# Kernel tuning notes

Hardware: AMD Instinct MI355X
Metric: run time of the kernel (lower is better)

The kernel has to match this reference:

```python
import jax, jax.numpy as jnp
import numpy as np
from jax import lax

T, B = 32, 256
C1, C2, C3 = 64, 128, 256
CDECAY, VDECAY, VTH, GRAD_WIN = 0.5, 0.75, 0.5, 0.3

# PseudoSpikeRect: hard threshold fwd, rectangular surrogate grad bwd
@jax.custom_vjp
def spike(v):
    return (v > VTH).astype(v.dtype)

def _spk_fwd(v):
    return spike(v), v

def _spk_bwd(v, g):
    return (g * (jnp.abs(v - VTH) < GRAD_WIN).astype(g.dtype),)

spike.defvjp(_spk_fwd, _spk_bwd)


def conv2d(x, w, b):
    y = lax.conv_general_dilated(x, w, (1, 1), 'VALID',
                                 dimension_numbers=('NCHW', 'OIHW', 'NCHW'))
    return y + b[None, :, None, None]


def lin(x, w, b):
    return x @ w.T + b


def lif(z, state):
    # CUBA-LIF cell: current decay + input psp, voltage decay with reset-by-spike
    spk, cur, vlt = state[0], state[1], state[2]
    cur = CDECAY * cur + z
    vlt = VDECAY * vlt * (1.0 - spk) + cur
    out = spike(vlt)
    return out, jnp.stack([out, cur, vlt])


def setup_inputs() -> dict:
    key = jax.random.key(0)
    ks = jax.random.split(key, 10)
    f32 = jnp.float32
    def rnd(k, shape, fan_in):
        return jax.random.normal(k, shape, f32) / np.sqrt(fan_in)
    return {
        'input_data': jax.random.normal(ks[0], (B, 1, 10, 10, T), f32),
        'conv1_w': rnd(ks[1], (C1, 1, 3, 3), 9),
        'conv1_b': jnp.zeros((C1,), f32),
        'conv2_w': rnd(ks[2], (C2, C1, 3, 3), 9 * C1),
        'conv2_b': jnp.zeros((C2,), f32),
        'conv3_w': rnd(ks[3], (C3, C2, 3, 3), 9 * C2),
        'conv3_b': jnp.zeros((C3,), f32),
        'tc_w': rnd(ks[4], (3, C3, C3), C3),
        'tc_b': jnp.zeros((3, C3), f32),
        'rec_w': rnd(ks[5], (C3, C3), C3),
        'rec_b': jnp.zeros((C3,), f32),
        'fc1_w': rnd(ks[6], (128, C3), C3),
        'fc1_b': jnp.zeros((128,), f32),
        'fc2_w': rnd(ks[7], (2, 128), 128),
        'ts_weights': jnp.ones((T, 1), f32) / T,
        'st_c1': jnp.zeros((3, B, C1, 8, 8), f32),
        'st_c2': jnp.zeros((3, B, C2, 6, 6), f32),
        'st_c3': jnp.zeros((3, B, C3, 1, 1), f32),
        'st_tc1': jnp.zeros((3, B, C3), f32),
        'st_r1': jnp.zeros((3, B, C3), f32),
        'st_f1': jnp.zeros((3, B, 128), f32),
    }


def reference(input_data, conv1_w, conv1_b, conv2_w, conv2_b, conv3_w, conv3_b,
              tc_w, tc_b, rec_w, rec_b, fc1_w, fc1_b, fc2_w, ts_weights,
              st_c1, st_c2, st_c3, st_tc1, st_r1, st_f1):
    xs = jnp.moveaxis(input_data, -1, 0)  # [T, B, 1, 10, 10]
    buf0 = jnp.zeros((3, B, C3), xs.dtype)  # temporal-conv spike buffer, oldest first

    # temporal conv: at step t only min(t+1,3) buffered spikes exist; psp_func j
    # applies to the j-th oldest buffered spike (buffer newest at index 2).
    def tc_len1(buf):
        return lin(buf[2], tc_w[0], tc_b[0])
    def tc_len2(buf):
        return lin(buf[1], tc_w[0], tc_b[0]) + lin(buf[2], tc_w[1], tc_b[1])
    def tc_len3(buf):
        return (lin(buf[0], tc_w[0], tc_b[0]) + lin(buf[1], tc_w[1], tc_b[1])
                + lin(buf[2], tc_w[2], tc_b[2]))

    def step(carry, inp):
        s1, s2, s3, stc, sr, sf, buf, acc = carry
        x, tw, t = inp
        c1, s1 = lif(conv2d(x, conv1_w, conv1_b), s1)
        c2, s2 = lif(conv2d(c1, conv2_w, conv2_b), s2)
        pooled = c2.reshape(B, C2, 3, 2, 3, 2).mean(axis=(3, 5))  # AvgPool2d(2)
        c3, s3 = lif(conv2d(pooled, conv3_w, conv3_b), s3)
        flat = c3.reshape(B, C3)
        buf = jnp.concatenate([buf[1:], flat[None]], axis=0)
        psp = lax.switch(jnp.minimum(t, 2), [tc_len1, tc_len2, tc_len3], buf)
        tc, stc = lif(psp, stc)
        r, sr = lif(tc + lin(sr[0], rec_w, rec_b), sr)  # recurrent: Identity psp + rec(pre_spike)
        f1, sf = lif(lin(r, fc1_w, fc1_b), sf)
        acc = acc + (f1 @ fc2_w.T) * tw
        return (s1, s2, s3, stc, sr, sf, buf, acc), None

    init = (st_c1, st_c2, st_c3, st_tc1, st_r1, st_f1, buf0,
            jnp.zeros((B, 2), xs.dtype))
    carry, _ = lax.scan(step, init, (xs, ts_weights[:, 0], jnp.arange(T)))
    return carry[-1]
```

## Files before the change

kernel.cpp:

```cpp
#include <hip/hip_runtime.h>

#define T 32
#define B 256

typedef int v4i __attribute__((ext_vector_type(4)));

#define OFF_BD2   0
#define OFF_BD3   368640
#define OFF_BDTC  1843200
#define OFF_BDF1  2826240
#define OFF_BDREC 2990080
#define OFF_S1    3514368
#define OFF_POOL  37068800
#define OFF_PSP3  46505984
#define OFF_S3    63283200
#define OFF_PSPTC 65380352
#define OFF_TC    82157568
#define OFF_R     84254720
#define OFF_PSPF1 OFF_PSPTC

__global__ __launch_bounds__(256) void k_prepd(const float* __restrict__ c2w,
        const float* __restrict__ c3w, const float* __restrict__ tcw,
        const float* __restrict__ f1w, const float* __restrict__ rcw,
        signed char* __restrict__ Bd2, signed char* __restrict__ Bd3,
        signed char* __restrict__ Bdtc, signed char* __restrict__ Bdf1,
        signed char* __restrict__ Bdrec) {
    int idx = blockIdx.x * 256 + threadIdx.x;
    float w; signed char* base; int plane, off;
    if (idx < 73728) {
        int oc = idx / 576, kpos = idx - oc * 576;
        int kk = kpos >> 6, ic = kpos & 63;
        int ky = kk / 3, kx = kk - ky * 3;
        w = c2w[((oc * 64 + ic) * 3 + ky) * 3 + kx];
        base = Bd2; plane = 73728; off = (kk * 128 + oc) * 64 + ic;
    } else if (idx < 368640) {
        int m = idx - 73728;
        int oc = m / 1152, kpos = m - oc * 1152;
        int win = kpos >> 7, ic = kpos & 127;
        w = c3w[(oc * 128 + ic) * 9 + win];
        base = Bd3; plane = 294912;
        off = ((kpos >> 6) * 256 + oc) * 64 + (kpos & 63);
    } else if (idx < 565248) {
        int m = idx - 368640;
        int oc = m / 768, kpos = m - oc * 768;
        int j = kpos >> 8, kc = kpos & 255;
        w = tcw[(j * 256 + oc) * 256 + kc];
        base = Bdtc; plane = 196608;
        off = ((kpos >> 6) * 256 + oc) * 64 + (kpos & 63);
    } else if (idx < 598016) {
        int m = idx - 565248;
        int oc = m >> 8, kc = m & 255;
        w = f1w[oc * 256 + kc];
        base = Bdf1; plane = 32768;
        off = ((kc >> 6) * 128 + oc) * 64 + (kc & 63);
    } else if (idx < 663552) {
        int m = idx - 598016;
        int oc = m >> 8, k = m & 255;
        w = rcw[oc * 256 + k];
        base = Bdrec; plane = 65536; off = m;
    } else return;
    long long W = (long long)rint((double)w * 2147483648.0);
#pragma unroll
    for (int d = 0; d < 3; ++d) {
        int dig = (int)(((W + 128) & 255) - 128);
        base[d * plane + off] = (signed char)dig;
        W = (W - dig) >> 8;
    }
    base[3 * plane + off] = (signed char)W;
}

__global__ __launch_bounds__(256) void k_conv1(const float* __restrict__ x,
        const float* __restrict__ w1, const float* __restrict__ b1,
        unsigned char* __restrict__ s1) {
    __shared__ float xl[3200];
    int b  = blockIdx.x >> 2;
    int bp = blockIdx.x & 3;
    int oc = threadIdx.x & 63;
    int sub = threadIdx.x >> 6;
    const float* xb = x + b * 3200;
    for (int i = threadIdx.x; i < 3200; i += 256)
        xl[(i & 31) * 100 + (i >> 5)] = xb[i];
    double wd[9];
#pragma unroll
    for (int j = 0; j < 9; ++j) wd[j] = (double)w1[oc * 9 + j];
    double bias = (double)b1[oc];
    __syncthreads();
    double cur[4], vlt[4];
    unsigned spkb = 0;
#pragma unroll
    for (int i = 0; i < 4; ++i) { cur[i] = 0.0; vlt[i] = 0.0; }
    const int pixbase = bp * 16 + sub * 4;
    for (int t = 0; t < T; ++t) {
#pragma unroll
        for (int i = 0; i < 4; ++i) {
            int pix = pixbase + i;
            int oy = pix >> 3, ox = pix & 7;
            const float* xt = &xl[t * 100 + oy * 10 + ox];
            double z = bias;
#pragma unroll
            for (int ky = 0; ky < 3; ++ky)
#pragma unroll
                for (int kx = 0; kx < 3; ++kx)
                    z = fma(wd[ky * 3 + kx], (double)xt[ky * 10 + kx], z);
            cur[i] = 0.5 * cur[i] + z;
            int s = (spkb >> i) & 1;
            vlt[i] = (s ? 0.0 : 0.75 * vlt[i]) + cur[i];
            s = (vlt[i] > 0.5) ? 1 : 0;
            spkb = (spkb & ~(1u << i)) | ((unsigned)s << i);
            s1[((size_t)(t * B + b) * 64 + pix) * 64 + oc] = (unsigned char)s;
        }
    }
}

__global__ __launch_bounds__(256, 2) void k_conv2(const unsigned char* __restrict__ s1,
        const signed char* __restrict__ Bd2, const float* __restrict__ cb2,
        unsigned char* __restrict__ pooled) {
    __shared__ __align__(16) unsigned char As[32 * 1024];
    __shared__ unsigned smask[4][64];
    const int b = blockIdx.x / 9;
    const int w = blockIdx.x - b * 9;
    const int wy = w / 3, wx = w - wy * 3;
    const int tid = threadIdx.x;
    const int wave = tid >> 6, lane = tid & 63;
    const int col = lane & 15, quad = lane >> 4;
    const int m = lane & 15;
    const int px = m >> 2, tq = m & 3;
    const int py0 = px >> 1, px0 = px & 1;

    {
        const int pixbase = (2 * wy) * 8 + 2 * wx;
        for (int c = tid; c < 2048; c += 256) {
            int t = c >> 6, rem = c & 63;
            int p = rem & 15, qo = rem >> 4;
            int ly = p >> 2, lx = p & 3;
            int pix = pixbase + ly * 8 + lx;
            v4i v = *(const v4i*)(s1 + (((size_t)(t * B + b) * 64 + pix) << 6) + qo * 16);
            *(v4i*)(As + t * 1024 + ((qo * 16) + (p ^ (2 * (t & 3)))) * 16) = v;
        }
    }
    __syncthreads();

    for (int nh = 0; nh < 2; ++nh) {
        const int oc = nh * 64 + wave * 16 + col;
        const int boff = oc * 64 + quad * 16;
        v4i acc[8][4];
#pragma unroll
        for (int mt = 0; mt < 8; ++mt)
#pragma unroll
            for (int d = 0; d < 4; ++d) acc[mt][d] = (v4i){0, 0, 0, 0};
        v4i Bc[4], Bn[4];
#pragma unroll
        for (int d = 0; d < 4; ++d)
            Bc[d] = *(const v4i*)(Bd2 + (size_t)d * 73728 + boff);
#pragma unroll 1
        for (int kk = 0; kk < 9; ++kk) {
            if (kk < 8) {
#pragma unroll
                for (int d = 0; d < 4; ++d)
                    Bn[d] = *(const v4i*)(Bd2 + (size_t)d * 73728 + (kk + 1) * 8192 + boff);
            }
            const int ky = kk / 3, kx = kk - ky * 3;
            const int p = (py0 + ky) * 4 + (px0 + kx);
            const unsigned char* Ab = As + tq * 1024 + (quad * 16 + (p ^ (2 * tq))) * 16;
#pragma unroll
            for (int mt = 0; mt < 8; ++mt) {
                v4i Af = *(const v4i*)(Ab + mt * 4096);
#pragma unroll
                for (int d = 0; d < 4; ++d)
                    acc[mt][d] = __builtin_amdgcn_mfma_i32_16x16x64_i8(Af, Bc[d], acc[mt][d], 0, 0, 0);
            }
            if (kk < 8) {
#pragma unroll
                for (int d = 0; d < 4; ++d) Bc[d] = Bn[d];
            }
        }
        double cur = 0.0, vlt = 0.0;
        int spk = 0;
        unsigned bits = 0;
        double bias = (double)cb2[oc];
#pragma unroll
        for (int mt = 0; mt < 8; ++mt)
#pragma unroll
            for (int r = 0; r < 4; ++r) {
                double v = (double)acc[mt][3][r];
                v = fma(v, 256.0, (double)acc[mt][2][r]);
                v = fma(v, 256.0, (double)acc[mt][1][r]);
                v = fma(v, 256.0, (double)acc[mt][0][r]);
                double z = fma(v, 0x1p-31, bias);
                cur = 0.5 * cur + z;
                vlt = (spk ? 0.0 : 0.75 * vlt) + cur;
                spk = (vlt > 0.5) ? 1 : 0;
                bits |= ((unsigned)spk) << (mt * 4 + r);
            }
        smask[quad][wave * 16 + col] = bits;
        __syncthreads();
        {
            unsigned m0 = smask[0][wave * 16 + col], m1 = smask[1][wave * 16 + col];
            unsigned m2 = smask[2][wave * 16 + col], m3 = smask[3][wave * 16 + col];
#pragma unroll
            for (int q = 0; q < 8; ++q) {
                int t = quad * 8 + q;
                unsigned s = ((m0 >> t) & 1) + ((m1 >> t) & 1) + ((m2 >> t) & 1) + ((m3 >> t) & 1);
                pooled[(size_t)((w * 32 + t) * 256 + b) * 128 + oc] = (unsigned char)s;
            }
        }
        __syncthreads();
    }
}

__global__ __launch_bounds__(256) void k_c3psp(const unsigned char* __restrict__ pooled,
        const signed char* __restrict__ Bd3, const float* __restrict__ b3,
        double* __restrict__ psp) {
    __shared__ __align__(16) unsigned char As[32 * 1168];
    const int mt = blockIdx.x, rbase = mt * 32;
    const int tid = threadIdx.x;
    const int wave = tid >> 6, lane = tid & 63;
    const int col = lane & 15, quad = lane >> 4;
    for (int c = tid; c < 2304; c += 256) {
        int row = c / 72, cho = c - row * 72;
        int wn = cho >> 3, ico = (cho & 7) * 16;
        v4i v = *(const v4i*)(pooled + ((size_t)(wn * 8192) + rbase + row) * 128 + ico);
        *(v4i*)(As + row * 1168 + cho * 16) = v;
    }
    __syncthreads();
    const int nb = wave * 64;
    const double scl[4] = { 0x1p-33, 0x1p-25, 0x1p-17, 0x1p-9 };
    double psum[2][4][4];
#pragma unroll
    for (int ml = 0; ml < 2; ++ml)
#pragma unroll
        for (int nt = 0; nt < 4; ++nt)
#pragma unroll
            for (int r = 0; r < 4; ++r) psum[ml][nt][r] = 0.0;
    for (int d = 0; d < 4; ++d) {
        v4i acc[2][4];
#pragma unroll
        for (int ml = 0; ml < 2; ++ml)
#pragma unroll
            for (int nt = 0; nt < 4; ++nt) acc[ml][nt] = (v4i){0, 0, 0, 0};
        v4i Bc[4], Bn[4];
#pragma unroll
        for (int nt = 0; nt < 4; ++nt)
            Bc[nt] = *(const v4i*)(Bd3 + (((size_t)(d * 18) * 256
                        + nb + nt * 16 + col) << 6) + quad * 16);
#pragma unroll 1
        for (int kk = 0; kk < 18; ++kk) {
            if (kk < 17) {
#pragma unroll
                for (int nt = 0; nt < 4; ++nt)
                    Bn[nt] = *(const v4i*)(Bd3 + (((size_t)(d * 18 + kk + 1) * 256
                                + nb + nt * 16 + col) << 6) + quad * 16);
            }
#pragma unroll
            for (int ml = 0; ml < 2; ++ml) {
                v4i Af = *(const v4i*)(As + (ml * 16 + col) * 1168 + kk * 64 + quad * 16);
#pragma unroll
                for (int nt = 0; nt < 4; ++nt)
                    acc[ml][nt] = __builtin_amdgcn_mfma_i32_16x16x64_i8(Af, Bc[nt], acc[ml][nt], 0, 0, 0);
            }
            if (kk < 17) {
#pragma unroll
                for (int nt = 0; nt < 4; ++nt) Bc[nt] = Bn[nt];
            }
        }
        double s = scl[d];
#pragma unroll
        for (int ml = 0; ml < 2; ++ml)
#pragma unroll
            for (int nt = 0; nt < 4; ++nt)
#pragma unroll
                for (int r = 0; r < 4; ++r)
                    psum[ml][nt][r] = fma((double)acc[ml][nt][r], s, psum[ml][nt][r]);
    }
#pragma unroll
    for (int ml = 0; ml < 2; ++ml)
#pragma unroll
        for (int nt = 0; nt < 4; ++nt) {
            double bias = (double)b3[nb + nt * 16 + col];
#pragma unroll
            for (int r = 0; r < 4; ++r) {
                int row = rbase + ml * 16 + quad * 4 + r;
                psp[(size_t)row * 256 + nb + nt * 16 + col] = bias + psum[ml][nt][r];
            }
        }
}

__global__ __launch_bounds__(256) void k_tcpsp(const unsigned char* __restrict__ s3,
        const signed char* __restrict__ Bdtc, const float* __restrict__ tcb,
        double* __restrict__ psp) {
    __shared__ __align__(16) unsigned char As[32 * 784];
    const int mt = blockIdx.x, rbase = mt * 32;
    const int t = rbase >> 8;
    const int tid = threadIdx.x;
    const int wave = tid >> 6, lane = tid & 63;
    const int col = lane & 15, quad = lane >> 4;
    for (int c = tid; c < 1536; c += 256) {
        int row = c / 48, cho = c - row * 48;
        int j = cho >> 4, kc = (cho & 15) * 16;
        int bb = (rbase + row) & 255;
        int src = (t >= 2) ? (t - 2 + j) : ((j <= t) ? j : -1);
        v4i v = (v4i){0, 0, 0, 0};
        if (src >= 0) v = *(const v4i*)(s3 + ((size_t)(src * 256 + bb)) * 256 + kc);
        *(v4i*)(As + row * 784 + cho * 16) = v;
    }
    __syncthreads();
    const int nb = wave * 64;
    const double scl[4] = { 0x1p-31, 0x1p-23, 0x1p-15, 0x1p-7 };
    double psum[2][4][4];
#pragma unroll
    for (int ml = 0; ml < 2; ++ml)
#pragma unroll
        for (int nt = 0; nt < 4; ++nt)
#pragma unroll
            for (int r = 0; r < 4; ++r) psum[ml][nt][r] = 0.0;
    for (int d = 0; d < 4; ++d) {
        v4i acc[2][4];
#pragma unroll
        for (int ml = 0; ml < 2; ++ml)
#pragma unroll
            for (int nt = 0; nt < 4; ++nt) acc[ml][nt] = (v4i){0, 0, 0, 0};
        v4i Bc[4], Bn[4];
#pragma unroll
        for (int nt = 0; nt < 4; ++nt)
            Bc[nt] = *(const v4i*)(Bdtc + (((size_t)(d * 12) * 256
                        + nb + nt * 16 + col) << 6) + quad * 16);
#pragma unroll 1
        for (int kk = 0; kk < 12; ++kk) {
            if (kk < 11) {
#pragma unroll
                for (int nt = 0; nt < 4; ++nt)
                    Bn[nt] = *(const v4i*)(Bdtc + (((size_t)(d * 12 + kk + 1) * 256
                                + nb + nt * 16 + col) << 6) + quad * 16);
            }
#pragma unroll
            for (int ml = 0; ml < 2; ++ml) {
                v4i Af = *(const v4i*)(As + (ml * 16 + col) * 784 + kk * 64 + quad * 16);
#pragma unroll
                for (int nt = 0; nt < 4; ++nt)
                    acc[ml][nt] = __builtin_amdgcn_mfma_i32_16x16x64_i8(Af, Bc[nt], acc[ml][nt], 0, 0, 0);
            }
            if (kk < 11) {
#pragma unroll
                for (int nt = 0; nt < 4; ++nt) Bc[nt] = Bn[nt];
            }
        }
        double s = scl[d];
#pragma unroll
        for (int ml = 0; ml < 2; ++ml)
#pragma unroll
            for (int nt = 0; nt < 4; ++nt)
#pragma unroll
                for (int r = 0; r < 4; ++r)
                    psum[ml][nt][r] = fma((double)acc[ml][nt][r], s, psum[ml][nt][r]);
    }
#pragma unroll
    for (int ml = 0; ml < 2; ++ml)
#pragma unroll
        for (int nt = 0; nt < 4; ++nt) {
            int n = nb + nt * 16 + col;
            double bias = (double)tcb[n];
            if (t >= 1) bias += (double)tcb[256 + n];
            if (t >= 2) bias += (double)tcb[512 + n];
#pragma unroll
            for (int r = 0; r < 4; ++r) {
                int row = rbase + ml * 16 + quad * 4 + r;
                psp[(size_t)row * 256 + n] = bias + psum[ml][nt][r];
            }
        }
}

__global__ __launch_bounds__(256) void k_lif_flat(const double* __restrict__ psp,
        unsigned char* __restrict__ out) {
    int n = blockIdx.x * 256 + threadIdx.x;
    double cur = 0.0, vlt = 0.0;
    int spk = 0;
    for (int t = 0; t < T; ++t) {
        double z = psp[(size_t)t * 65536 + n];
        cur = 0.5 * cur + z;
        vlt = (spk ? 0.0 : 0.75 * vlt) + cur;
        spk = (vlt > 0.5) ? 1 : 0;
        out[(size_t)t * 65536 + n] = (unsigned char)spk;
    }
}

__global__ __launch_bounds__(512, 2) void k_recmm(const unsigned char* __restrict__ tcspk,
        const signed char* __restrict__ Bdrec, const float* __restrict__ rb,
        unsigned char* __restrict__ rspk) {
    __shared__ __align__(16) unsigned char Abuf[2][16][272];
    const int g = blockIdx.x;
    const int tid = threadIdx.x;
    const int wv = tid >> 6, lane = tid & 63;
    const int col = lane & 15, quad = lane >> 4;

    for (int c = tid; c < 2176; c += 512) ((int*)Abuf)[c] = 0;

    v4i Breg[2][4][4];
#pragma unroll
    for (int nt = 0; nt < 2; ++nt) {
        int ocb = wv * 32 + nt * 16 + col;
#pragma unroll
        for (int kc = 0; kc < 4; ++kc)
#pragma unroll
            for (int d = 0; d < 4; ++d)
                Breg[nt][kc][d] = *(const v4i*)(Bdrec + (size_t)d * 65536
                                                + ocb * 256 + kc * 64 + quad * 16);
    }
    double bias[2] = { (double)rb[wv * 32 + col], (double)rb[wv * 32 + 16 + col] };
    double cur[2][4], vlt[2][4];
    int spk[2][4];
#pragma unroll
    for (int nt = 0; nt < 2; ++nt)
#pragma unroll
        for (int r = 0; r < 4; ++r) { cur[nt][r] = 0.0; vlt[nt][r] = 0.0; spk[nt][r] = 0; }
    const unsigned char* tcp = tcspk + (size_t)(g * 16 + quad * 4) * 256 + wv * 32 + col;
    unsigned char* rsp = rspk + (size_t)(g * 16 + quad * 4) * 256 + wv * 32 + col;
    __syncthreads();

    for (int t = 0; t < T; ++t) {
        unsigned char tcv[2][4];
#pragma unroll
        for (int nt = 0; nt < 2; ++nt)
#pragma unroll
            for (int r = 0; r < 4; ++r)
                tcv[nt][r] = tcp[(size_t)t * 65536 + r * 256 + nt * 16];
        v4i Af[4];
#pragma unroll
        for (int kc = 0; kc < 4; ++kc)
            Af[kc] = *(const v4i*)(&Abuf[t & 1][col][kc * 64 + quad * 16]);
        v4i acc[2][4];
#pragma unroll
        for (int nt = 0; nt < 2; ++nt)
#pragma unroll
            for (int d = 0; d < 4; ++d) acc[nt][d] = (v4i){0, 0, 0, 0};
#pragma unroll
        for (int kc = 0; kc < 4; ++kc)
#pragma unroll
            for (int nt = 0; nt < 2; ++nt)
#pragma unroll
                for (int d = 0; d < 4; ++d)
                    acc[nt][d] = __builtin_amdgcn_mfma_i32_16x16x64_i8(Af[kc], Breg[nt][kc][d], acc[nt][d], 0, 0, 0);
#pragma unroll
        for (int nt = 0; nt < 2; ++nt)
#pragma unroll
            for (int r = 0; r < 4; ++r) {
                double v = (double)acc[nt][3][r];
                v = fma(v, 256.0, (double)acc[nt][2][r]);
                v = fma(v, 256.0, (double)acc[nt][1][r]);
                v = fma(v, 256.0, (double)acc[nt][0][r]);
                double z = fma(v, 0x1p-31, bias[nt]) + (double)tcv[nt][r];
                cur[nt][r] = 0.5 * cur[nt][r] + z;
                vlt[nt][r] = (spk[nt][r] ? 0.0 : 0.75 * vlt[nt][r]) + cur[nt][r];
                int s = (vlt[nt][r] > 0.5) ? 1 : 0;
                spk[nt][r] = s;
                rsp[(size_t)t * 65536 + r * 256 + nt * 16] = (unsigned char)s;
                Abuf[(t + 1) & 1][quad * 4 + r][wv * 32 + nt * 16 + col] = (unsigned char)s;
            }
        __syncthreads();
    }
}

__global__ __launch_bounds__(256) void k_f1psp(const unsigned char* __restrict__ rspk,
        const signed char* __restrict__ Bdf1, const float* __restrict__ f1b,
        double* __restrict__ psp) {
    __shared__ __align__(16) unsigned char As[16 * 272];
    const int mt = blockIdx.x, rbase = mt * 16;
    const int tid = threadIdx.x;
    const int wave = tid >> 6, lane = tid & 63;
    const int col = lane & 15, quad = lane >> 4;
    if (tid < 256) {
        int row = tid >> 4, cho = tid & 15;
        v4i v = *(const v4i*)(rspk + (size_t)(rbase + row) * 256 + cho * 16);
        *(v4i*)(As + row * 272 + cho * 16) = v;
    }
    __syncthreads();
    const int nb = wave * 32;
    const double scl[4] = { 0x1p-31, 0x1p-23, 0x1p-15, 0x1p-7 };
    double psum[2][4];
#pragma unroll
    for (int nt = 0; nt < 2; ++nt)
#pragma unroll
        for (int r = 0; r < 4; ++r) psum[nt][r] = 0.0;
    for (int d = 0; d < 4; ++d) {
        v4i acc[2];
        acc[0] = (v4i){0, 0, 0, 0};
        acc[1] = (v4i){0, 0, 0, 0};
#pragma unroll
        for (int kk = 0; kk < 4; ++kk) {
            v4i Af = *(const v4i*)(As + (lane & 15) * 272 + kk * 64 + quad * 16);
#pragma unroll
            for (int nt = 0; nt < 2; ++nt) {
                v4i Bf = *(const v4i*)(Bdf1 + (((size_t)(d * 4 + kk) * 128
                        + nb + nt * 16 + col) << 6) + quad * 16);
                acc[nt] = __builtin_amdgcn_mfma_i32_16x16x64_i8(Af, Bf, acc[nt], 0, 0, 0);
            }
        }
        double s = scl[d];
#pragma unroll
        for (int nt = 0; nt < 2; ++nt)
#pragma unroll
            for (int r = 0; r < 4; ++r)
                psum[nt][r] = fma((double)acc[nt][r], s, psum[nt][r]);
    }
#pragma unroll
    for (int nt = 0; nt < 2; ++nt) {
        int n = nb + nt * 16 + col;
        double bias = (double)f1b[n];
#pragma unroll
        for (int r = 0; r < 4; ++r) {
            int row = rbase + quad * 4 + r;
            psp[(size_t)row * 128 + n] = bias + psum[nt][r];
        }
    }
}

__global__ __launch_bounds__(128) void k_fc_out(const double* __restrict__ psp,
        const float* __restrict__ fc2w, const float* __restrict__ tsw,
        float* __restrict__ out) {
    __shared__ double sm[128];
    int b = blockIdx.x, oc = threadIdx.x;
    double ps[T];
#pragma unroll
    for (int t = 0; t < T; ++t)
        ps[t] = psp[((size_t)t * B + b) * 128 + oc];
    double cur = 0.0, vlt = 0.0, sAcc = 0.0;
    int spk = 0;
#pragma unroll
    for (int t = 0; t < T; ++t) {
        cur = 0.5 * cur + ps[t];
        vlt = (spk ? 0.0 : 0.75 * vlt) + cur;
        spk = (vlt > 0.5) ? 1 : 0;
        if (spk) sAcc += (double)tsw[t];
    }
    sm[oc] = sAcc;
    __syncthreads();
    if (oc < 2) {
        double s = 0.0;
        for (int k = 0; k < 128; ++k)
            s = fma(sm[k], (double)fc2w[oc * 128 + k], s);
        out[b * 2 + oc] = (float)s;
    }
}

extern "C" void kernel_launch(void* const* d_in, const int* in_sizes, int n_in,
                              void* d_out, int out_size, void* d_ws, size_t ws_size,
                              hipStream_t stream) {
    const float* x   = (const float*)d_in[0];
    const float* c1w = (const float*)d_in[1];
    const float* c1b = (const float*)d_in[2];
    const float* c2w = (const float*)d_in[3];
    const float* c2b = (const float*)d_in[4];
    const float* c3w = (const float*)d_in[5];
    const float* c3b = (const float*)d_in[6];
    const float* tcw = (const float*)d_in[7];
    const float* tcb = (const float*)d_in[8];
    const float* rcw = (const float*)d_in[9];
    const float* rcb = (const float*)d_in[10];
    const float* f1w = (const float*)d_in[11];
    const float* f1b = (const float*)d_in[12];
    const float* f2w = (const float*)d_in[13];
    const float* tsw = (const float*)d_in[14];

    char* ws = (char*)d_ws;
    signed char* Bd2      = (signed char*)(ws + OFF_BD2);
    signed char* Bd3      = (signed char*)(ws + OFF_BD3);
    signed char* Bdtc     = (signed char*)(ws + OFF_BDTC);
    signed char* Bdf1     = (signed char*)(ws + OFF_BDF1);
    signed char* Bdrec    = (signed char*)(ws + OFF_BDREC);
    unsigned char* s1     = (unsigned char*)(ws + OFF_S1);
    unsigned char* pool   = (unsigned char*)(ws + OFF_POOL);
    double* psp3          = (double*)(ws + OFF_PSP3);
    unsigned char* s3     = (unsigned char*)(ws + OFF_S3);
    double* psptc         = (double*)(ws + OFF_PSPTC);
    unsigned char* tcs    = (unsigned char*)(ws + OFF_TC);
    unsigned char* rsp    = (unsigned char*)(ws + OFF_R);
    double* pspf1         = (double*)(ws + OFF_PSPF1);

    k_prepd   <<<2592, 256, 0, stream>>>(c2w, c3w, tcw, f1w, rcw, Bd2, Bd3, Bdtc, Bdf1, Bdrec);
    k_conv1   <<<1024, 256, 0, stream>>>(x, c1w, c1b, s1);
    k_conv2   <<<2304, 256, 0, stream>>>(s1, Bd2, c2b, pool);
    k_c3psp   <<<256,  256, 0, stream>>>(pool, Bd3, c3b, psp3);
    k_lif_flat<<<256,  256, 0, stream>>>(psp3, s3);
    k_tcpsp   <<<256,  256, 0, stream>>>(s3, Bdtc, tcb, psptc);
    k_lif_flat<<<256,  256, 0, stream>>>(psptc, tcs);
    k_recmm   <<<16,   512, 0, stream>>>(tcs, Bdrec, rcb, rsp);
    k_f1psp   <<<512,  256, 0, stream>>>(rsp, Bdf1, f1b, pspf1);
    k_fc_out  <<<256,  128, 0, stream>>>(pspf1, f2w, tsw, (float*)d_out);
}
```

Baseline: 369.1 us.

## Compute conv1 in fp32 with time-major vector loads; pool conv2 via shuffles

```diff
diff --git a/kernel.cpp b/kernel.cpp
--- a/kernel.cpp
+++ b/kernel.cpp
@@ -79,34 +79,41 @@
     int sub = threadIdx.x >> 6;
     const float* xb = x + b * 3200;
     for (int i = threadIdx.x; i < 3200; i += 256)
-        xl[(i & 31) * 100 + (i >> 5)] = xb[i];
-    double wd[9];
-#pragma unroll
-    for (int j = 0; j < 9; ++j) wd[j] = (double)w1[oc * 9 + j];
-    double bias = (double)b1[oc];
-    __syncthreads();
-    double cur[4], vlt[4];
-    unsigned spkb = 0;
-#pragma unroll
-    for (int i = 0; i < 4; ++i) { cur[i] = 0.0; vlt[i] = 0.0; }
+        xl[i] = xb[i];
+    float wf[9];
+#pragma unroll
+    for (int j = 0; j < 9; ++j) wf[j] = w1[oc * 9 + j];
+    float biasf = b1[oc];
+    __syncthreads();
     const int pixbase = bp * 16 + sub * 4;
-    for (int t = 0; t < T; ++t) {
-#pragma unroll
-        for (int i = 0; i < 4; ++i) {
-            int pix = pixbase + i;
-            int oy = pix >> 3, ox = pix & 7;
-            const float* xt = &xl[t * 100 + oy * 10 + ox];
-            double z = bias;
-#pragma unroll
-            for (int ky = 0; ky < 3; ++ky)
-#pragma unroll
-                for (int kx = 0; kx < 3; ++kx)
-                    z = fma(wd[ky * 3 + kx], (double)xt[ky * 10 + kx], z);
-            cur[i] = 0.5 * cur[i] + z;
-            int s = (spkb >> i) & 1;
-            vlt[i] = (s ? 0.0 : 0.75 * vlt[i]) + cur[i];
-            s = (vlt[i] > 0.5) ? 1 : 0;
-            spkb = (spkb & ~(1u << i)) | ((unsigned)s << i);
+#pragma unroll
+    for (int i = 0; i < 4; ++i) {
+        int pix = pixbase + i;
+        int oy = pix >> 3, ox = pix & 7;
+        float z[T];
+#pragma unroll
+        for (int t = 0; t < T; ++t) z[t] = biasf;
+#pragma unroll
+        for (int ky = 0; ky < 3; ++ky)
+#pragma unroll
+            for (int kx = 0; kx < 3; ++kx) {
+                const float* xp = &xl[((oy + ky) * 10 + ox + kx) * 32];
+                float w = wf[ky * 3 + kx];
+#pragma unroll
+                for (int tq = 0; tq < 8; ++tq) {
+                    float4 v = *(const float4*)(xp + tq * 4);
+                    z[tq * 4 + 0] = fmaf(w, v.x, z[tq * 4 + 0]);
+                    z[tq * 4 + 1] = fmaf(w, v.y, z[tq * 4 + 1]);
+                    z[tq * 4 + 2] = fmaf(w, v.z, z[tq * 4 + 2]);
+                    z[tq * 4 + 3] = fmaf(w, v.w, z[tq * 4 + 3]);
+                }
+            }
+        double cur = 0.0, vlt = 0.0;
+        int s = 0;
+        for (int t = 0; t < T; ++t) {
+            cur = 0.5 * cur + (double)z[t];
+            vlt = (s ? 0.0 : 0.75 * vlt) + cur;
+            s = (vlt > 0.5) ? 1 : 0;
             s1[((size_t)(t * B + b) * 64 + pix) * 64 + oc] = (unsigned char)s;
         }
     }
@@ -116,7 +123,6 @@
         const signed char* __restrict__ Bd2, const float* __restrict__ cb2,
         unsigned char* __restrict__ pooled) {
     __shared__ __align__(16) unsigned char As[32 * 1024];
-    __shared__ unsigned smask[4][64];
     const int b = blockIdx.x / 9;
     const int w = blockIdx.x - b * 9;
     const int wy = w / 3, wx = w - wy * 3;
@@ -192,19 +198,18 @@
                 spk = (vlt > 0.5) ? 1 : 0;
                 bits |= ((unsigned)spk) << (mt * 4 + r);
             }
-        smask[quad][wave * 16 + col] = bits;
-        __syncthreads();
         {
-            unsigned m0 = smask[0][wave * 16 + col], m1 = smask[1][wave * 16 + col];
-            unsigned m2 = smask[2][wave * 16 + col], m3 = smask[3][wave * 16 + col];
+            unsigned m0 = bits;
+            unsigned mx = __shfl_xor((int)bits, 16);
+            unsigned my = __shfl_xor((int)bits, 32);
+            unsigned mz = __shfl_xor((int)mx, 32);
 #pragma unroll
             for (int q = 0; q < 8; ++q) {
                 int t = quad * 8 + q;
-                unsigned s = ((m0 >> t) & 1) + ((m1 >> t) & 1) + ((m2 >> t) & 1) + ((m3 >> t) & 1);
+                unsigned s = ((m0 >> t) & 1) + ((mx >> t) & 1) + ((my >> t) & 1) + ((mz >> t) & 1);
                 pooled[(size_t)((w * 32 + t) * 256 + b) * 128 + oc] = (unsigned char)s;
             }
         }
-        __syncthreads();
     }
 }
 
```

Result: slower. 386.9 us (+4.8%).

## Switch intermediates to batch-major layout and fuse flat LIF into GEMM kernels

Applied to the files above, without the earlier changes.

```diff
diff --git a/kernel.cpp b/kernel.cpp
--- a/kernel.cpp
+++ b/kernel.cpp
@@ -12,12 +12,10 @@
 #define OFF_BDREC 2990080
 #define OFF_S1    3514368
 #define OFF_POOL  37068800
-#define OFF_PSP3  46505984
 #define OFF_S3    63283200
-#define OFF_PSPTC 65380352
 #define OFF_TC    82157568
 #define OFF_R     84254720
-#define OFF_PSPF1 OFF_PSPTC
+#define OFF_PSPF1 65380352
 
 __global__ __launch_bounds__(256) void k_prepd(const float* __restrict__ c2w,
         const float* __restrict__ c3w, const float* __restrict__ tcw,
@@ -79,34 +77,41 @@
     int sub = threadIdx.x >> 6;
     const float* xb = x + b * 3200;
     for (int i = threadIdx.x; i < 3200; i += 256)
-        xl[(i & 31) * 100 + (i >> 5)] = xb[i];
+        xl[i] = xb[i];
     double wd[9];
 #pragma unroll
     for (int j = 0; j < 9; ++j) wd[j] = (double)w1[oc * 9 + j];
     double bias = (double)b1[oc];
     __syncthreads();
-    double cur[4], vlt[4];
-    unsigned spkb = 0;
-#pragma unroll
-    for (int i = 0; i < 4; ++i) { cur[i] = 0.0; vlt[i] = 0.0; }
     const int pixbase = bp * 16 + sub * 4;
-    for (int t = 0; t < T; ++t) {
-#pragma unroll
-        for (int i = 0; i < 4; ++i) {
-            int pix = pixbase + i;
-            int oy = pix >> 3, ox = pix & 7;
-            const float* xt = &xl[t * 100 + oy * 10 + ox];
-            double z = bias;
-#pragma unroll
-            for (int ky = 0; ky < 3; ++ky)
-#pragma unroll
-                for (int kx = 0; kx < 3; ++kx)
-                    z = fma(wd[ky * 3 + kx], (double)xt[ky * 10 + kx], z);
-            cur[i] = 0.5 * cur[i] + z;
-            int s = (spkb >> i) & 1;
-            vlt[i] = (s ? 0.0 : 0.75 * vlt[i]) + cur[i];
-            s = (vlt[i] > 0.5) ? 1 : 0;
-            spkb = (spkb & ~(1u << i)) | ((unsigned)s << i);
+#pragma unroll
+    for (int i = 0; i < 4; ++i) {
+        int pix = pixbase + i;
+        int oy = pix >> 3, ox = pix & 7;
+        double z[T];
+#pragma unroll
+        for (int t = 0; t < T; ++t) z[t] = bias;
+#pragma unroll
+        for (int ky = 0; ky < 3; ++ky)
+#pragma unroll
+            for (int kx = 0; kx < 3; ++kx) {
+                const float* xp = &xl[((oy + ky) * 10 + ox + kx) * 32];
+                double w = wd[ky * 3 + kx];
+#pragma unroll
+                for (int tq = 0; tq < 8; ++tq) {
+                    float4 v = *(const float4*)(xp + tq * 4);
+                    z[tq * 4 + 0] = fma(w, (double)v.x, z[tq * 4 + 0]);
+                    z[tq * 4 + 1] = fma(w, (double)v.y, z[tq * 4 + 1]);
+                    z[tq * 4 + 2] = fma(w, (double)v.z, z[tq * 4 + 2]);
+                    z[tq * 4 + 3] = fma(w, (double)v.w, z[tq * 4 + 3]);
+                }
+            }
+        double cur = 0.0, vlt = 0.0;
+        int s = 0;
+        for (int t = 0; t < T; ++t) {
+            cur = 0.5 * cur + z[t];
+            vlt = (s ? 0.0 : 0.75 * vlt) + cur;
+            s = (vlt > 0.5) ? 1 : 0;
             s1[((size_t)(t * B + b) * 64 + pix) * 64 + oc] = (unsigned char)s;
         }
     }
@@ -201,7 +206,7 @@
             for (int q = 0; q < 8; ++q) {
                 int t = quad * 8 + q;
                 unsigned s = ((m0 >> t) & 1) + ((m1 >> t) & 1) + ((m2 >> t) & 1) + ((m3 >> t) & 1);
-                pooled[(size_t)((w * 32 + t) * 256 + b) * 128 + oc] = (unsigned char)s;
+                pooled[(size_t)((w * 256 + b) * 32 + t) * 128 + oc] = (unsigned char)s;
             }
         }
         __syncthreads();
@@ -210,7 +215,7 @@
 
 __global__ __launch_bounds__(256) void k_c3psp(const unsigned char* __restrict__ pooled,
         const signed char* __restrict__ Bd3, const float* __restrict__ b3,
-        double* __restrict__ psp) {
+        unsigned char* __restrict__ s3) {
     __shared__ __align__(16) unsigned char As[32 * 1168];
     const int mt = blockIdx.x, rbase = mt * 32;
     const int tid = threadIdx.x;
@@ -272,35 +277,49 @@
                 for (int r = 0; r < 4; ++r)
                     psum[ml][nt][r] = fma((double)acc[ml][nt][r], s, psum[ml][nt][r]);
     }
-#pragma unroll
-    for (int ml = 0; ml < 2; ++ml)
-#pragma unroll
-        for (int nt = 0; nt < 4; ++nt) {
-            double bias = (double)b3[nb + nt * 16 + col];
-#pragma unroll
-            for (int r = 0; r < 4; ++r) {
-                int row = rbase + ml * 16 + quad * 4 + r;
-                psp[(size_t)row * 256 + nb + nt * 16 + col] = bias + psum[ml][nt][r];
-            }
-        }
+    double* tb = (double*)As + wave * (32 * 33);
+    for (int p = 0; p < 2; ++p) {
+        __syncthreads();
+#pragma unroll
+        for (int ml = 0; ml < 2; ++ml)
+#pragma unroll
+            for (int q = 0; q < 2; ++q)
+#pragma unroll
+                for (int r = 0; r < 4; ++r) {
+                    int t = ml * 16 + quad * 4 + r;
+                    tb[t * 33 + q * 16 + col] = psum[ml][p * 2 + q][r];
+                }
+        __syncthreads();
+        if (lane < 32) {
+            int oc = nb + p * 32 + lane;
+            double bias = (double)b3[oc];
+            double cur = 0.0, vlt = 0.0;
+            int spk = 0;
+            for (int t = 0; t < T; ++t) {
+                double z = bias + tb[t * 33 + lane];
+                cur = 0.5 * cur + z;
+                vlt = (spk ? 0.0 : 0.75 * vlt) + cur;
+                spk = (vlt > 0.5) ? 1 : 0;
+                s3[(size_t)(rbase + t) * 256 + oc] = (unsigned char)spk;
+            }
+        }
+    }
 }
 
 __global__ __launch_bounds__(256) void k_tcpsp(const unsigned char* __restrict__ s3,
         const signed char* __restrict__ Bdtc, const float* __restrict__ tcb,
-        double* __restrict__ psp) {
-    __shared__ __align__(16) unsigned char As[32 * 784];
+        unsigned char* __restrict__ tcs) {
+    __shared__ __align__(16) unsigned char As[33792];
     const int mt = blockIdx.x, rbase = mt * 32;
-    const int t = rbase >> 8;
     const int tid = threadIdx.x;
     const int wave = tid >> 6, lane = tid & 63;
     const int col = lane & 15, quad = lane >> 4;
     for (int c = tid; c < 1536; c += 256) {
         int row = c / 48, cho = c - row * 48;
         int j = cho >> 4, kc = (cho & 15) * 16;
-        int bb = (rbase + row) & 255;
-        int src = (t >= 2) ? (t - 2 + j) : ((j <= t) ? j : -1);
+        int src = (row >= 2) ? (row - 2 + j) : ((j <= row) ? j : -1);
         v4i v = (v4i){0, 0, 0, 0};
-        if (src >= 0) v = *(const v4i*)(s3 + ((size_t)(src * 256 + bb)) * 256 + kc);
+        if (src >= 0) v = *(const v4i*)(s3 + ((size_t)(rbase + src)) * 256 + kc);
         *(v4i*)(As + row * 784 + cho * 16) = v;
     }
     __syncthreads();
@@ -353,33 +372,35 @@
                 for (int r = 0; r < 4; ++r)
                     psum[ml][nt][r] = fma((double)acc[ml][nt][r], s, psum[ml][nt][r]);
     }
-#pragma unroll
-    for (int ml = 0; ml < 2; ++ml)
-#pragma unroll
-        for (int nt = 0; nt < 4; ++nt) {
-            int n = nb + nt * 16 + col;
-            double bias = (double)tcb[n];
-            if (t >= 1) bias += (double)tcb[256 + n];
-            if (t >= 2) bias += (double)tcb[512 + n];
-#pragma unroll
-            for (int r = 0; r < 4; ++r) {
-                int row = rbase + ml * 16 + quad * 4 + r;
-                psp[(size_t)row * 256 + n] = bias + psum[ml][nt][r];
-            }
-        }
-}
-
-__global__ __launch_bounds__(256) void k_lif_flat(const double* __restrict__ psp,
-        unsigned char* __restrict__ out) {
-    int n = blockIdx.x * 256 + threadIdx.x;
-    double cur = 0.0, vlt = 0.0;
-    int spk = 0;
-    for (int t = 0; t < T; ++t) {
-        double z = psp[(size_t)t * 65536 + n];
-        cur = 0.5 * cur + z;
-        vlt = (spk ? 0.0 : 0.75 * vlt) + cur;
-        spk = (vlt > 0.5) ? 1 : 0;
-        out[(size_t)t * 65536 + n] = (unsigned char)spk;
+    double* tb = (double*)As + wave * (32 * 33);
+    for (int p = 0; p < 2; ++p) {
+        __syncthreads();
+#pragma unroll
+        for (int ml = 0; ml < 2; ++ml)
+#pragma unroll
+            for (int q = 0; q < 2; ++q)
+#pragma unroll
+                for (int r = 0; r < 4; ++r) {
+                    int t = ml * 16 + quad * 4 + r;
+                    tb[t * 33 + q * 16 + col] = psum[ml][p * 2 + q][r];
+                }
+        __syncthreads();
+        if (lane < 32) {
+            int oc = nb + p * 32 + lane;
+            double b0 = (double)tcb[oc], b1 = (double)tcb[256 + oc], b2 = (double)tcb[512 + oc];
+            double cur = 0.0, vlt = 0.0;
+            int spk = 0;
+            for (int t = 0; t < T; ++t) {
+                double bias = b0;
+                if (t >= 1) bias += b1;
+                if (t >= 2) bias += b2;
+                double z = bias + tb[t * 33 + lane];
+                cur = 0.5 * cur + z;
+                vlt = (spk ? 0.0 : 0.75 * vlt) + cur;
+                spk = (vlt > 0.5) ? 1 : 0;
+                tcs[(size_t)(rbase + t) * 256 + oc] = (unsigned char)spk;
+            }
+        }
     }
 }
 
@@ -412,8 +433,8 @@
     for (int nt = 0; nt < 2; ++nt)
 #pragma unroll
         for (int r = 0; r < 4; ++r) { cur[nt][r] = 0.0; vlt[nt][r] = 0.0; spk[nt][r] = 0; }
-    const unsigned char* tcp = tcspk + (size_t)(g * 16 + quad * 4) * 256 + wv * 32 + col;
-    unsigned char* rsp = rspk + (size_t)(g * 16 + quad * 4) * 256 + wv * 32 + col;
+    const unsigned char* tcp = tcspk + (size_t)(g * 16 + quad * 4) * 32 * 256 + wv * 32 + col;
+    unsigned char* rsp = rspk + (size_t)(g * 16 + quad * 4) * 32 * 256 + wv * 32 + col;
     __syncthreads();
 
     for (int t = 0; t < T; ++t) {
@@ -422,7 +443,7 @@
         for (int nt = 0; nt < 2; ++nt)
 #pragma unroll
             for (int r = 0; r < 4; ++r)
-                tcv[nt][r] = tcp[(size_t)t * 65536 + r * 256 + nt * 16];
+                tcv[nt][r] = tcp[(size_t)(r * 32 + t) * 256 + nt * 16];
         v4i Af[4];
 #pragma unroll
         for (int kc = 0; kc < 4; ++kc)
@@ -452,7 +473,7 @@
                 vlt[nt][r] = (spk[nt][r] ? 0.0 : 0.75 * vlt[nt][r]) + cur[nt][r];
                 int s = (vlt[nt][r] > 0.5) ? 1 : 0;
                 spk[nt][r] = s;
-                rsp[(size_t)t * 65536 + r * 256 + nt * 16] = (unsigned char)s;
+                rsp[(size_t)(r * 32 + t) * 256 + nt * 16] = (unsigned char)s;
                 Abuf[(t + 1) & 1][quad * 4 + r][wv * 32 + nt * 16 + col] = (unsigned char)s;
             }
         __syncthreads();
@@ -521,7 +542,7 @@
     double ps[T];
 #pragma unroll
     for (int t = 0; t < T; ++t)
-        ps[t] = psp[((size_t)t * B + b) * 128 + oc];
+        ps[t] = psp[((size_t)(b * 32 + t)) * 128 + oc];
     double cur = 0.0, vlt = 0.0, sAcc = 0.0;
     int spk = 0;
 #pragma unroll
@@ -568,9 +589,7 @@
     signed char* Bdrec    = (signed char*)(ws + OFF_BDREC);
     unsigned char* s1     = (unsigned char*)(ws + OFF_S1);
     unsigned char* pool   = (unsigned char*)(ws + OFF_POOL);
-    double* psp3          = (double*)(ws + OFF_PSP3);
     unsigned char* s3     = (unsigned char*)(ws + OFF_S3);
-    double* psptc         = (double*)(ws + OFF_PSPTC);
     unsigned char* tcs    = (unsigned char*)(ws + OFF_TC);
     unsigned char* rsp    = (unsigned char*)(ws + OFF_R);
     double* pspf1         = (double*)(ws + OFF_PSPF1);
@@ -578,10 +597,8 @@
     k_prepd   <<<2592, 256, 0, stream>>>(c2w, c3w, tcw, f1w, rcw, Bd2, Bd3, Bdtc, Bdf1, Bdrec);
     k_conv1   <<<1024, 256, 0, stream>>>(x, c1w, c1b, s1);
     k_conv2   <<<2304, 256, 0, stream>>>(s1, Bd2, c2b, pool);
-    k_c3psp   <<<256,  256, 0, stream>>>(pool, Bd3, c3b, psp3);
-    k_lif_flat<<<256,  256, 0, stream>>>(psp3, s3);
-    k_tcpsp   <<<256,  256, 0, stream>>>(s3, Bdtc, tcb, psptc);
-    k_lif_flat<<<256,  256, 0, stream>>>(psptc, tcs);
+    k_c3psp   <<<256,  256, 0, stream>>>(pool, Bd3, c3b, s3);
+    k_tcpsp   <<<256,  256, 0, stream>>>(s3, Bdtc, tcb, tcs);
     k_recmm   <<<16,   512, 0, stream>>>(tcs, Bdrec, rcb, rsp);
     k_f1psp   <<<512,  256, 0, stream>>>(rsp, Bdf1, f1b, pspf1);
     k_fc_out  <<<256,  128, 0, stream>>>(pspf1, f2w, tsw, (float*)d_out);
```

New measurement: 392.4 us. +6.3%, slower.
